# Performance work log

Hardware: AMD Instinct MI355X
Metric: run time of the kernel (lower is better)

Reference implementation:

```python
import jax, jax.numpy as jnp
import numpy as np

B, T, D, H = 4, 2048, 1024, 16
DK = D // H


def setup_inputs() -> dict:
    key = jax.random.key(0)
    ks = jax.random.split(key, 9)
    s = 1.0 / np.sqrt(D)
    x = jax.random.normal(ks[0], (B, T, D), dtype=jnp.float32)
    # causal mask: 1 = keep, 0 = masked (broadcastable over batch and heads)
    mask = jnp.tril(jnp.ones((T, T), dtype=jnp.int32))[None, None]
    params = {}
    for i, name in enumerate(['Wq', 'Wk', 'Wv', 'Wo']):
        params[name] = jax.random.normal(ks[1 + i], (D, D), dtype=jnp.float32) * s
    for i, name in enumerate(['bq', 'bk', 'bv', 'bo']):
        params[name] = jax.random.normal(ks[5 + i], (D,), dtype=jnp.float32) * s
    return {'x': x, 'mask': mask, **params}


def reference(x, mask, Wq, Wk, Wv, Wo, bq, bk, bv, bo):
    Bn, Tn, Dn = x.shape
    # torch.nn.Linear: y = x @ W.T + b
    q = (x @ Wq.T + bq).reshape(Bn, Tn, H, DK).transpose(0, 2, 1, 3)  # [B,H,T,dk]
    k = (x @ Wk.T + bk).reshape(Bn, Tn, H, DK).transpose(0, 2, 1, 3)
    v = (x @ Wv.T + bv).reshape(Bn, Tn, H, DK).transpose(0, 2, 1, 3)
    scores = jnp.einsum('bhqd,bhkd->bhqk', q, k) / jnp.sqrt(jnp.float32(DK))
    scores = jnp.where(mask == 0, -jnp.inf, scores)
    attn = jax.nn.softmax(scores, axis=-1)
    out = jnp.einsum('bhqk,bhkd->bhqd', attn, v)  # [B,H,T,dk]
    out = out.transpose(0, 2, 1, 3).reshape(Bn, Tn, Dn)
    return out @ Wo.T + bo
```

## Files before the change

kernel.cpp:

```cpp
#include <hip/hip_runtime.h>
#include <hip/hip_bf16.h>

#define T_LEN 2048
#define D_DIM 1024
#define H_NUM 16
#define DK 64

typedef unsigned short u16;
typedef __bf16 bf16x8 __attribute__((ext_vector_type(8)));
typedef float f32x4 __attribute__((ext_vector_type(4)));
typedef u16 u16x8 __attribute__((ext_vector_type(8)));
typedef u16 u16x4 __attribute__((ext_vector_type(4)));

#define AS1 __attribute__((address_space(1)))
#define AS3 __attribute__((address_space(3)))

#define QSCALE 0.18033688011112042f

__device__ __forceinline__ u16 f2bf(float f) {
    unsigned u = __builtin_bit_cast(unsigned, f);
    unsigned rounding = 0x7FFFu + ((u >> 16) & 1u);
    return (u16)((u + rounding) >> 16);
}

__global__ __launch_bounds__(256) void cvt_bf16(const float* __restrict__ in,
                                                u16* __restrict__ out, int n8) {
    int i = blockIdx.x * blockDim.x + threadIdx.x;
    if (i >= n8) return;
    const float4* p = (const float4*)in + (size_t)i * 2;
    float4 a = p[0], b = p[1];
    u16x8 r;
    r[0] = f2bf(a.x); r[1] = f2bf(a.y); r[2] = f2bf(a.z); r[3] = f2bf(a.w);
    r[4] = f2bf(b.x); r[5] = f2bf(b.y); r[6] = f2bf(b.z); r[7] = f2bf(b.w);
    *((u16x8*)out + i) = r;
}

__global__ __launch_bounds__(256) void cvt4_bf16(const float* __restrict__ a,
                                                 const float* __restrict__ b,
                                                 const float* __restrict__ c,
                                                 const float* __restrict__ d,
                                                 u16* __restrict__ out, int n8per) {
    int s = blockIdx.y;
    const float* src = s == 0 ? a : (s == 1 ? b : (s == 2 ? c : d));
    int i = blockIdx.x * blockDim.x + threadIdx.x;
    if (i >= n8per) return;
    const float4* p = (const float4*)src + (size_t)i * 2;
    float4 x = p[0], y = p[1];
    u16x8 r;
    r[0] = f2bf(x.x); r[1] = f2bf(x.y); r[2] = f2bf(x.z); r[3] = f2bf(x.w);
    r[4] = f2bf(y.x); r[5] = f2bf(y.y); r[6] = f2bf(y.z); r[7] = f2bf(y.w);
    *((u16x8*)(out + (size_t)s * n8per * 8) + i) = r;
}

template <int MODE>
__global__ __launch_bounds__(256) void gemm_bt(const u16* __restrict__ A,
                                               const u16* __restrict__ W,
                                               const float* __restrict__ b0,
                                               const float* __restrict__ b1,
                                               const float* __restrict__ b2,
                                               void* __restrict__ Cout,
                                               int M, int N, int K,
                                               int nxt, int nyt) {
    __shared__ u16 lA[2][128 * 32];
    __shared__ u16 lB[2][128 * 32];
    const int tid = threadIdx.x;
    const int w = tid >> 6, lane = tid & 63;

    const int bid = blockIdx.x;
    const int idx = bid >> 3;
    const int y = idx % nyt;
    const int x = (bid & 7) * (nxt >> 3) + idx / nyt;
    const int tm = x * 128;
    const int tn = y * 128;

    const int wm = (w >> 1) * 64, wn = (w & 1) * 64;
    const int kgrp = (lane >> 4) * 8;

    f32x4 acc[4][4] = {};

    auto stage = [&](int buf, int k0) {
#pragma unroll
        for (int r = 0; r < 2; ++r) {
            int c = r * 256 + tid;
            int row = c >> 2, col = (c & 3) * 8;
            __builtin_amdgcn_global_load_lds(
                (AS1 const void*)(A + (size_t)(tm + row) * K + k0 + col),
                (AS3 void*)(&lA[buf][(r * 256 + w * 64) * 8]), 16, 0, 0);
            __builtin_amdgcn_global_load_lds(
                (AS1 const void*)(W + (size_t)(tn + row) * K + k0 + col),
                (AS3 void*)(&lB[buf][(r * 256 + w * 64) * 8]), 16, 0, 0);
        }
    };

    stage(0, 0);
    asm volatile("s_waitcnt vmcnt(0)" ::: "memory");
    __syncthreads();

    const int niter = K >> 5;
    for (int it = 0; it < niter; ++it) {
        const int cur = it & 1;
        if (it + 1 < niter) stage(cur ^ 1, (it + 1) << 5);

        bf16x8 af[4], bfr[4];
#pragma unroll
        for (int i = 0; i < 4; ++i) {
            af[i]  = *(const bf16x8*)(&lA[cur][(wm + i * 16 + (lane & 15)) * 32 + kgrp]);
            bfr[i] = *(const bf16x8*)(&lB[cur][(wn + i * 16 + (lane & 15)) * 32 + kgrp]);
        }
#pragma unroll
        for (int mi = 0; mi < 4; ++mi)
#pragma unroll
            for (int ni = 0; ni < 4; ++ni)
                acc[mi][ni] = __builtin_amdgcn_mfma_f32_16x16x32_bf16(
                    af[mi], bfr[ni], acc[mi][ni], 0, 0, 0);

        asm volatile("s_waitcnt vmcnt(0)" ::: "memory");
        __syncthreads();
    }

    const int mtx = tn >> 10;
    const float* bp = mtx == 0 ? b0 : (mtx == 1 ? b1 : b2);
    const int crow0 = (lane >> 4) * 4;
    const int ccol = lane & 15;
#pragma unroll
    for (int mi = 0; mi < 4; ++mi) {
#pragma unroll
        for (int ni = 0; ni < 4; ++ni) {
            int n = tn + wn + ni * 16 + ccol;
            float bv = bp[n & 1023];
#pragma unroll
            for (int r = 0; r < 4; ++r) {
                int m = tm + wm + mi * 16 + crow0 + r;
                float val = acc[mi][ni][r] + bv;
                if (MODE == 0) {
                    ((float*)Cout)[(size_t)m * N + n] = val;
                } else {
                    if (mtx == 0) val *= QSCALE;
                    int b = m >> 11, t = m & (T_LEN - 1);
                    int nn = n & 1023;
                    int h = nn >> 6, d = nn & 63;
                    ((u16*)Cout)[(size_t)mtx * 8388608 +
                                 ((size_t)(b * H_NUM + h) * T_LEN + t) * DK + d] = f2bf(val);
                }
            }
        }
    }
}

__global__ __launch_bounds__(512) void attn_fwd(const u16* __restrict__ q,
                                                const u16* __restrict__ k,
                                                const u16* __restrict__ v,
                                                u16* __restrict__ o) {
    __shared__ u16 lK[2][64 * 64];
    __shared__ u16 lV[2][64 * 64];
    __shared__ u16 lP[8][16 * 72];
    __shared__ float lSc[8][16];

    const int tid = threadIdx.x, w = tid >> 6, lane = tid & 63;
    const int bid = blockIdx.x;
    const int idx = bid >> 3;
    const int bh = (bid & 7) * 8 + (idx & 7);
    const int bx = idx >> 3;

    const u16* qb = q + (size_t)bh * T_LEN * DK;
    const u16* kb = k + (size_t)bh * T_LEN * DK;
    const u16* vb = v + (size_t)bh * T_LEN * DK;

    const int g = lane >> 4;
    const int ccol = lane & 15;
    const int kg = tid >> 4;
    const int dc = tid & 15;
    const int wk = w - 4;
    const int b_ = bh >> 4, h_ = bh & 15;

    for (int seg = 0; seg < 2; ++seg) {
        const int qblk = seg ? (15 - bx) : bx;
        const int q0 = qblk * 128;
        const int ntiles = 2 * qblk + 2;
        const int rowbase = q0 + w * 16;
        const int myq = rowbase + ccol;

        bf16x8 qa[2];
#pragma unroll
        for (int kk = 0; kk < 2; ++kk)
            qa[kk] = *(const bf16x8*)(qb + (size_t)(rowbase + ccol) * DK + kk * 32 + g * 8);

        f32x4 oacc[4] = {};
        float mrow = -1e30f, lpart = 0.f;

        u16x4 vr[4];
        if (w >= 4) {
#pragma unroll
            for (int r2 = 0; r2 < 2; ++r2) {
                int c = r2 * 256 + wk * 64 + lane;
                int row = c >> 3, ch = c & 7;
                __builtin_amdgcn_global_load_lds(
                    (AS1 const void*)(kb + (size_t)row * DK + (ch ^ (row & 7)) * 8),
                    (AS3 void*)(&lK[0][(r2 * 256 + wk * 64) * 8]), 16, 0, 0);
            }
        } else {
#pragma unroll
            for (int i = 0; i < 4; ++i)
                vr[i] = *(const u16x4*)(vb + (size_t)(kg * 4 + i) * DK + dc * 4);
        }

        for (int kt = 0; kt < ntiles; ++kt) {
            const int bf = kt & 1;
            const int kv0 = kt << 6;
            asm volatile("s_waitcnt vmcnt(0)" ::: "memory");
            if (w < 4) {
#pragma unroll
                for (int j = 0; j < 4; ++j) {
                    int d = dc * 4 + j;
                    u16x4 t4;
                    t4[0] = vr[0][j]; t4[1] = vr[1][j]; t4[2] = vr[2][j]; t4[3] = vr[3][j];
                    *(u16x4*)(&lV[bf][d * 64 +
                        (((kg >> 1) ^ ((d >> 1) & 7)) * 8 + (kg & 1) * 4)]) = t4;
                }
            }
            __syncthreads();

            if (kt + 1 < ntiles) {
                const int kvn = (kt + 1) << 6;
                if (w >= 4) {
#pragma unroll
                    for (int r2 = 0; r2 < 2; ++r2) {
                        int c = r2 * 256 + wk * 64 + lane;
                        int row = c >> 3, ch = c & 7;
                        __builtin_amdgcn_global_load_lds(
                            (AS1 const void*)(kb + (size_t)(kvn + row) * DK + (ch ^ (row & 7)) * 8),
                            (AS3 void*)(&lK[bf ^ 1][(r2 * 256 + wk * 64) * 8]), 16, 0, 0);
                    }
                } else {
#pragma unroll
                    for (int i = 0; i < 4; ++i)
                        vr[i] = *(const u16x4*)(vb + (size_t)(kvn + kg * 4 + i) * DK + dc * 4);
                }
            }

            if (kv0 < rowbase + 16) {
                f32x4 sacc[4] = {};
                __builtin_amdgcn_s_setprio(1);
#pragma unroll
                for (int nt = 0; nt < 4; ++nt)
#pragma unroll
                    for (int kk = 0; kk < 2; ++kk) {
                        bf16x8 kf = *(const bf16x8*)(&lK[bf][(nt * 16 + ccol) * 64 +
                                                     (((kk * 4 + g) ^ (ccol & 7)) * 8)]);
                        sacc[nt] = __builtin_amdgcn_mfma_f32_16x16x32_bf16(
                            kf, qa[kk], sacc[nt], 0, 0, 0);
                    }
                __builtin_amdgcn_s_setprio(0);

                const bool full = (kv0 + 63) <= rowbase;
                float mx = -1e30f;
#pragma unroll
                for (int nt = 0; nt < 4; ++nt)
#pragma unroll
                    for (int r = 0; r < 4; ++r) {
                        float sv = sacc[nt][r];
                        if (!full && (kv0 + nt * 16 + g * 4 + r > myq)) sv = -1e30f;
                        sacc[nt][r] = sv;
                        mx = fmaxf(mx, sv);
                    }
                mx = fmaxf(mx, __shfl_xor(mx, 16));
                mx = fmaxf(mx, __shfl_xor(mx, 32));

                const bool skiprow = (mx <= mrow + 8.f);
                float mnew = skiprow ? mrow : mx;
                float p[4][4];
                float rsl = 0.f;
#pragma unroll
                for (int nt = 0; nt < 4; ++nt)
#pragma unroll
                    for (int r = 0; r < 4; ++r) {
                        float pv = __builtin_amdgcn_exp2f(sacc[nt][r] - mnew);
                        p[nt][r] = pv;
                        rsl += pv;
                    }
                float scal = skiprow ? 1.f : __builtin_amdgcn_exp2f(mrow - mnew);
                lpart = lpart * scal + rsl;
                mrow = mnew;

                if (lane < 16) lSc[w][lane] = scal;
#pragma unroll
                for (int nt = 0; nt < 4; ++nt) {
                    u16x4 t4;
                    t4[0] = f2bf(p[nt][0]); t4[1] = f2bf(p[nt][1]);
                    t4[2] = f2bf(p[nt][2]); t4[3] = f2bf(p[nt][3]);
                    *(u16x4*)(&lP[w][ccol * 72 + nt * 16 + g * 4]) = t4;
                }
                asm volatile("s_waitcnt lgkmcnt(0)" ::: "memory");

                f32x4 scalC = *(const f32x4*)(&lSc[w][g * 4]);
                if (__any(!skiprow)) {
#pragma unroll
                    for (int nt2 = 0; nt2 < 4; ++nt2)
#pragma unroll
                        for (int r = 0; r < 4; ++r) oacc[nt2][r] *= scalC[r];
                }

                bf16x8 pa[2];
#pragma unroll
                for (int kk2 = 0; kk2 < 2; ++kk2)
                    pa[kk2] = *(const bf16x8*)(&lP[w][ccol * 72 + kk2 * 32 + g * 8]);

                const int vsw = (ccol >> 1) & 7;
                __builtin_amdgcn_s_setprio(1);
#pragma unroll
                for (int nt2 = 0; nt2 < 4; ++nt2) {
#pragma unroll
                    for (int kk2 = 0; kk2 < 2; ++kk2) {
                        bf16x8 vf = *(const bf16x8*)(&lV[bf][(nt2 * 16 + ccol) * 64 +
                                                     (((kk2 * 4 + g) ^ vsw) * 8)]);
                        oacc[nt2] = __builtin_amdgcn_mfma_f32_16x16x32_bf16(
                            pa[kk2], vf, oacc[nt2], 0, 0, 0);
                    }
                }
                __builtin_amdgcn_s_setprio(0);
            }
        }
        __syncthreads();

        float rs = lpart;
        rs += __shfl_xor(rs, 16);
        rs += __shfl_xor(rs, 32);
        if (lane < 16) lSc[w][lane] = rs;
        asm volatile("s_waitcnt lgkmcnt(0)" ::: "memory");
        f32x4 rsC = *(const f32x4*)(&lSc[w][g * 4]);
#pragma unroll
        for (int r = 0; r < 4; ++r) {
            float inv = 1.0f / rsC[r];
            int trow = rowbase + g * 4 + r;
#pragma unroll
            for (int nt2 = 0; nt2 < 4; ++nt2) {
                float val = oacc[nt2][r] * inv;
                o[(size_t)(b_ * T_LEN + trow) * D_DIM + h_ * DK + nt2 * 16 + ccol] = f2bf(val);
            }
        }
        __syncthreads();
    }
}

extern "C" void kernel_launch(void* const* d_in, const int* in_sizes, int n_in,
                              void* d_out, int out_size, void* d_ws, size_t ws_size,
                              hipStream_t stream) {
    const float* x  = (const float*)d_in[0];
    const float* Wq = (const float*)d_in[2];
    const float* Wk = (const float*)d_in[3];
    const float* Wv = (const float*)d_in[4];
    const float* Wo = (const float*)d_in[5];
    const float* bq = (const float*)d_in[6];
    const float* bk = (const float*)d_in[7];
    const float* bv = (const float*)d_in[8];
    const float* bo = (const float*)d_in[9];

    char* ws = (char*)d_ws;
    u16* xb   = (u16*)(ws);
    u16* wqb  = (u16*)(ws + 16777216);
    u16* wob  = (u16*)(ws + 23068672);
    u16* qws  = (u16*)(ws + 25165824);
    u16* kws  = (u16*)(ws + 41943040);
    u16* vws  = (u16*)(ws + 58720256);
    u16* attnb = xb;

    cvt_bf16<<<4096, 256, 0, stream>>>(x, xb, 1048576);
    cvt4_bf16<<<dim3(512, 4), 256, 0, stream>>>(Wq, Wk, Wv, Wo, wqb, 131072);

    gemm_bt<1><<<1536, 256, 0, stream>>>(xb, wqb, bq, bk, bv, qws, 8192, 3072, 1024, 64, 24);

    attn_fwd<<<512, 512, 0, stream>>>(qws, kws, vws, attnb);

    gemm_bt<0><<<512, 256, 0, stream>>>(attnb, wob, bo, bo, bo, d_out, 8192, 1024, 1024, 64, 8);
}
```

Baseline: 291.8 us.

## Add dedicated 256x256-tile QKV GEMM with swizzled LDS and deeper prefetch

Replaces the generic 128x128 QKV projection GEMM with a dedicated 512-thread kernel that computes 256x256 output tiles. It uses direct global-to-LDS loads, an XOR-swizzled LDS layout, and a multi-stage pipeline of half-k sub-tiles interleaved with MFMA phases under raised wave priority. The goal is more operand reuse per LDS byte, fewer bank conflicts, and better overlap of loads with compute. The trade-offs are more registers (128 accumulators per thread) and only 384 blocks, which may leave CUs underfilled. The output-projection GEMM is reduced to a plain fp32-output version with the mode template removed.

```diff
diff --git a/kernel.cpp b/kernel.cpp
--- a/kernel.cpp
+++ b/kernel.cpp
@@ -52,13 +52,116 @@
     *((u16x8*)(out + (size_t)s * n8per * 8) + i) = r;
 }
 
-template <int MODE>
+__global__ __launch_bounds__(512) void gemm_qkv(const u16* __restrict__ A,
+                                                const u16* __restrict__ W,
+                                                const float* __restrict__ b0,
+                                                const float* __restrict__ b1,
+                                                const float* __restrict__ b2,
+                                                u16* __restrict__ Cout) {
+    __shared__ u16 L[2][4][8192];
+    const int tid = threadIdx.x, w = tid >> 6, lane = tid & 63;
+    const int sw = (blockIdx.x & 7) * 48 + (blockIdx.x >> 3);
+    const int xm = sw / 12, yn = sw % 12;
+    const int tm = xm * 256, tn = yn * 256;
+    const int wr = w >> 2, wc = w & 3;
+    const int g = lane >> 4, ccol = lane & 15;
+    const int gsw = (g ^ ((ccol >> 1) & 3)) * 8;
+    const int K = 1024, NT = 16;
+
+    const u16* Ab = A + (size_t)tm * K;
+    const u16* Wb = W + (size_t)tn * K;
+
+    const int srow = w * 16 + (lane >> 2);
+    const int skk  = (((lane & 3) ^ ((lane >> 3) & 3))) * 8;
+
+    f32x4 acc[8][4] = {};
+
+    auto stage = [&](const u16* gb, int k0, int ksub, u16* reg) {
+#pragma unroll
+        for (int h2 = 0; h2 < 2; ++h2) {
+            __builtin_amdgcn_global_load_lds(
+                (AS1 const void*)(gb + (size_t)(h2 * 128 + srow) * K + k0 + ksub * 32 + skk),
+                (AS3 void*)(reg + h2 * 4096 + w * 512), 16, 0, 0);
+        }
+    };
+
+    stage(Ab, 0, 0, L[0][0]);
+    stage(Wb, 0, 0, L[0][2]);
+    stage(Ab, 0, 1, L[0][1]);
+    stage(Wb, 0, 1, L[0][3]);
+    stage(Ab, 64, 0, L[1][0]);
+    stage(Wb, 64, 0, L[1][2]);
+    asm volatile("s_waitcnt vmcnt(4)" ::: "memory");
+    __builtin_amdgcn_s_barrier();
+
+    bf16x8 bfr[4];
+    for (int t = 0; t < NT; ++t) {
+        const int par = t & 1;
+        u16* LA0 = L[par][0]; u16* LA1 = L[par][1];
+        u16* LB0 = L[par][2]; u16* LB1 = L[par][3];
+#pragma unroll
+        for (int p = 0; p < 4; ++p) {
+            const int mh = (p & 1) * 4;
+            u16* LAk = (p >> 1) ? LA1 : LA0;
+            u16* LBk = (p >> 1) ? LB1 : LB0;
+            bf16x8 af[4];
+#pragma unroll
+            for (int i = 0; i < 4; ++i)
+                af[i] = *(const bf16x8*)(LAk + (wr * 128 + (mh + i) * 16 + ccol) * 32 + gsw);
+            if ((p & 1) == 0) {
+#pragma unroll
+                for (int i = 0; i < 4; ++i)
+                    bfr[i] = *(const bf16x8*)(LBk + (wc * 64 + i * 16 + ccol) * 32 + gsw);
+            }
+            if (p == 0)      { if (t + 1 < NT) stage(Ab, (t + 1) * 64, 1, L[(t + 1) & 1][1]); }
+            else if (p == 1) { if (t + 1 < NT) stage(Wb, (t + 1) * 64, 1, L[(t + 1) & 1][3]); }
+            else if (p == 2) { if (t + 2 < NT) stage(Ab, (t + 2) * 64, 0, L[par][0]); }
+            else {
+                if (t + 2 < NT) stage(Wb, (t + 2) * 64, 0, L[par][2]);
+                if (t < NT - 2) asm volatile("s_waitcnt vmcnt(4)" ::: "memory");
+                else            asm volatile("s_waitcnt vmcnt(0)" ::: "memory");
+            }
+            __builtin_amdgcn_s_barrier();
+            asm volatile("s_waitcnt lgkmcnt(0)" ::: "memory");
+            __builtin_amdgcn_sched_barrier(0);
+            __builtin_amdgcn_s_setprio(1);
+#pragma unroll
+            for (int ni = 0; ni < 4; ++ni)
+#pragma unroll
+                for (int mi = 0; mi < 4; ++mi)
+                    acc[mh + mi][ni] = __builtin_amdgcn_mfma_f32_16x16x32_bf16(
+                        af[mi], bfr[ni], acc[mh + mi][ni], 0, 0, 0);
+            __builtin_amdgcn_s_setprio(0);
+            __builtin_amdgcn_s_barrier();
+        }
+    }
+
+    const int mtx = yn >> 2;
+    const float* bp = mtx == 0 ? b0 : (mtx == 1 ? b1 : b2);
+#pragma unroll
+    for (int mi = 0; mi < 8; ++mi) {
+#pragma unroll
+        for (int ni = 0; ni < 4; ++ni) {
+            int nn = (tn + wc * 64 + ni * 16 + ccol) & 1023;
+            float bv = bp[nn];
+            int h = nn >> 6, d = nn & 63;
+#pragma unroll
+            for (int r = 0; r < 4; ++r) {
+                int m = tm + wr * 128 + mi * 16 + g * 4 + r;
+                float val = acc[mi][ni][r] + bv;
+                if (mtx == 0) val *= QSCALE;
+                int b = m >> 11, tt = m & (T_LEN - 1);
+                Cout[(size_t)mtx * 8388608 +
+                     ((size_t)(b * H_NUM + h) * T_LEN + tt) * DK + d] = f2bf(val);
+            }
+        }
+    }
+}
+
 __global__ __launch_bounds__(256) void gemm_bt(const u16* __restrict__ A,
                                                const u16* __restrict__ W,
                                                const float* __restrict__ b0,
-                                               const float* __restrict__ b1,
-                                               const float* __restrict__ b2,
-                                               void* __restrict__ Cout,
+                                               float* __restrict__ Cout,
                                                int M, int N, int K,
                                                int nxt, int nyt) {
     __shared__ u16 lA[2][128 * 32];
@@ -118,8 +221,6 @@
         __syncthreads();
     }
 
-    const int mtx = tn >> 10;
-    const float* bp = mtx == 0 ? b0 : (mtx == 1 ? b1 : b2);
     const int crow0 = (lane >> 4) * 4;
     const int ccol = lane & 15;
 #pragma unroll
@@ -127,21 +228,11 @@
 #pragma unroll
         for (int ni = 0; ni < 4; ++ni) {
             int n = tn + wn + ni * 16 + ccol;
-            float bv = bp[n & 1023];
+            float bv = b0[n & 1023];
 #pragma unroll
             for (int r = 0; r < 4; ++r) {
                 int m = tm + wm + mi * 16 + crow0 + r;
-                float val = acc[mi][ni][r] + bv;
-                if (MODE == 0) {
-                    ((float*)Cout)[(size_t)m * N + n] = val;
-                } else {
-                    if (mtx == 0) val *= QSCALE;
-                    int b = m >> 11, t = m & (T_LEN - 1);
-                    int nn = n & 1023;
-                    int h = nn >> 6, d = nn & 63;
-                    ((u16*)Cout)[(size_t)mtx * 8388608 +
-                                 ((size_t)(b * H_NUM + h) * T_LEN + t) * DK + d] = f2bf(val);
-                }
+                Cout[(size_t)m * N + n] = acc[mi][ni][r] + bv;
             }
         }
     }
@@ -367,9 +458,9 @@
     cvt_bf16<<<4096, 256, 0, stream>>>(x, xb, 1048576);
     cvt4_bf16<<<dim3(512, 4), 256, 0, stream>>>(Wq, Wk, Wv, Wo, wqb, 131072);
 
-    gemm_bt<1><<<1536, 256, 0, stream>>>(xb, wqb, bq, bk, bv, qws, 8192, 3072, 1024, 64, 24);
+    gemm_qkv<<<384, 512, 0, stream>>>(xb, wqb, bq, bk, bv, qws);
 
     attn_fwd<<<512, 512, 0, stream>>>(qws, kws, vws, attnb);
 
-    gemm_bt<0><<<512, 256, 0, stream>>>(attnb, wob, bo, bo, bo, d_out, 8192, 1024, 1024, 64, 8);
-}
+    gemm_bt<<<512, 256, 0, stream>>>(attnb, wob, bo, (float*)d_out, 8192, 1024, 1024, 64, 8);
+}
```

Result: faster. 273.5 us (-6.3%).

## Rewrite projection GEMMs with 128x256 tiles, deeper LDS pipeline and swizzle

Applied to the files above, without the earlier changes.

Replaces the 128x128, 256-thread GEMM with a 512-thread kernel computing 128x256 tiles. Each K step of 64 is split into two 32-wide phases, and loads are kept about three stages ahead using counted vmcnt waits. LDS reads are XOR-swizzled to cut bank conflicts, and MFMA priority is raised. The attention kernel also switches P conversion to the hardware packed bf16 convert instruction. The cost is more LDS per block, which lowers occupancy, and hardcoded K and N dimensions.

```diff
diff --git a/kernel.cpp b/kernel.cpp
--- a/kernel.cpp
+++ b/kernel.cpp
@@ -52,76 +52,91 @@
     *((u16x8*)(out + (size_t)s * n8per * 8) + i) = r;
 }
 
-template <int MODE>
-__global__ __launch_bounds__(256) void gemm_bt(const u16* __restrict__ A,
+template <int MODE, int NYT>
+__global__ __launch_bounds__(512) void gemm_bp(const u16* __restrict__ A,
                                                const u16* __restrict__ W,
                                                const float* __restrict__ b0,
                                                const float* __restrict__ b1,
                                                const float* __restrict__ b2,
-                                               void* __restrict__ Cout,
-                                               int M, int N, int K,
-                                               int nxt, int nyt) {
-    __shared__ u16 lA[2][128 * 32];
-    __shared__ u16 lB[2][128 * 32];
-    const int tid = threadIdx.x;
-    const int w = tid >> 6, lane = tid & 63;
-
-    const int bid = blockIdx.x;
-    const int idx = bid >> 3;
-    const int y = idx % nyt;
-    const int x = (bid & 7) * (nxt >> 3) + idx / nyt;
-    const int tm = x * 128;
-    const int tn = y * 128;
-
-    const int wm = (w >> 1) * 64, wn = (w & 1) * 64;
-    const int kgrp = (lane >> 4) * 8;
+                                               void* __restrict__ Cout) {
+    __shared__ u16 LA[2][2][4096];
+    __shared__ u16 LB[2][2][8192];
+    const int tid = threadIdx.x, w = tid >> 6, lane = tid & 63;
+    const int loc = blockIdx.x >> 3;
+    const int xm = (blockIdx.x & 7) * 8 + loc / NYT;
+    const int yn = loc % NYT;
+    const int tm = xm * 128, tn = yn * 256;
+    const int wr = w >> 2, wc = w & 3;
+    const int wm = wr * 64, wn = wc * 64;
+    const int g = lane >> 4, ccol = lane & 15;
+    const int gsw = (g ^ ((ccol >> 1) & 3)) * 8;
+    const int NT = 16;
+
+    const int srow = tid >> 2;
+    const int skk = ((tid & 3) ^ ((tid >> 3) & 3)) * 8;
 
     f32x4 acc[4][4] = {};
 
-    auto stage = [&](int buf, int k0) {
-#pragma unroll
-        for (int r = 0; r < 2; ++r) {
-            int c = r * 256 + tid;
-            int row = c >> 2, col = (c & 3) * 8;
+    auto stageA = [&](int par, int kk, int k0) {
+        __builtin_amdgcn_global_load_lds(
+            (AS1 const void*)(A + (size_t)(tm + srow) * 1024 + k0 + kk * 32 + skk),
+            (AS3 void*)(&LA[par][kk][w * 512]), 16, 0, 0);
+    };
+    auto stageB = [&](int par, int kk, int k0) {
+#pragma unroll
+        for (int h = 0; h < 2; ++h)
             __builtin_amdgcn_global_load_lds(
-                (AS1 const void*)(A + (size_t)(tm + row) * K + k0 + col),
-                (AS3 void*)(&lA[buf][(r * 256 + w * 64) * 8]), 16, 0, 0);
-            __builtin_amdgcn_global_load_lds(
-                (AS1 const void*)(W + (size_t)(tn + row) * K + k0 + col),
-                (AS3 void*)(&lB[buf][(r * 256 + w * 64) * 8]), 16, 0, 0);
-        }
+                (AS1 const void*)(W + (size_t)(tn + h * 128 + srow) * 1024 + k0 + kk * 32 + skk),
+                (AS3 void*)(&LB[par][kk][h * 4096 + w * 512]), 16, 0, 0);
     };
 
-    stage(0, 0);
-    asm volatile("s_waitcnt vmcnt(0)" ::: "memory");
-    __syncthreads();
-
-    const int niter = K >> 5;
-    for (int it = 0; it < niter; ++it) {
-        const int cur = it & 1;
-        if (it + 1 < niter) stage(cur ^ 1, (it + 1) << 5);
-
-        bf16x8 af[4], bfr[4];
-#pragma unroll
-        for (int i = 0; i < 4; ++i) {
-            af[i]  = *(const bf16x8*)(&lA[cur][(wm + i * 16 + (lane & 15)) * 32 + kgrp]);
-            bfr[i] = *(const bf16x8*)(&lB[cur][(wn + i * 16 + (lane & 15)) * 32 + kgrp]);
-        }
-#pragma unroll
-        for (int mi = 0; mi < 4; ++mi)
-#pragma unroll
-            for (int ni = 0; ni < 4; ++ni)
-                acc[mi][ni] = __builtin_amdgcn_mfma_f32_16x16x32_bf16(
-                    af[mi], bfr[ni], acc[mi][ni], 0, 0, 0);
-
-        asm volatile("s_waitcnt vmcnt(0)" ::: "memory");
-        __syncthreads();
+    stageA(0, 0, 0);  stageB(0, 0, 0);
+    stageA(0, 1, 0);  stageB(0, 1, 0);
+    stageA(1, 0, 64); stageB(1, 0, 64);
+
+    for (int t = 0; t < NT; ++t) {
+        const int par = t & 1;
+#pragma unroll
+        for (int ph = 0; ph < 2; ++ph) {
+            if (ph == 0) {
+                if (t + 1 < NT) { stageA(par ^ 1, 1, (t + 1) * 64); stageB(par ^ 1, 1, (t + 1) * 64); }
+            } else {
+                if (t + 2 < NT) { stageA(par, 0, (t + 2) * 64); stageB(par, 0, (t + 2) * 64); }
+            }
+            if (ph == 0) {
+                if (t < NT - 1) asm volatile("s_waitcnt vmcnt(9)" ::: "memory");
+                else            asm volatile("s_waitcnt vmcnt(3)" ::: "memory");
+            } else {
+                if (t < NT - 2)      asm volatile("s_waitcnt vmcnt(9)" ::: "memory");
+                else if (t == NT - 2) asm volatile("s_waitcnt vmcnt(6)" ::: "memory");
+                else                 asm volatile("s_waitcnt vmcnt(0)" ::: "memory");
+            }
+            __builtin_amdgcn_s_barrier();
+
+            const u16* LAp = LA[par][ph];
+            const u16* LBp = LB[par][ph];
+            bf16x8 af[4], bfr[4];
+#pragma unroll
+            for (int i = 0; i < 4; ++i) {
+                af[i]  = *(const bf16x8*)(LAp + (wm + i * 16 + ccol) * 32 + gsw);
+                bfr[i] = *(const bf16x8*)(LBp + (wn + i * 16 + ccol) * 32 + gsw);
+            }
+            asm volatile("s_waitcnt lgkmcnt(0)" ::: "memory");
+            __builtin_amdgcn_sched_barrier(0);
+            __builtin_amdgcn_s_setprio(1);
+#pragma unroll
+            for (int mi = 0; mi < 4; ++mi)
+#pragma unroll
+                for (int ni = 0; ni < 4; ++ni)
+                    acc[mi][ni] = __builtin_amdgcn_mfma_f32_16x16x32_bf16(
+                        af[mi], bfr[ni], acc[mi][ni], 0, 0, 0);
+            __builtin_amdgcn_s_setprio(0);
+            __builtin_amdgcn_s_barrier();
+        }
     }
 
-    const int mtx = tn >> 10;
-    const float* bp = mtx == 0 ? b0 : (mtx == 1 ? b1 : b2);
-    const int crow0 = (lane >> 4) * 4;
-    const int ccol = lane & 15;
+    const int mtx = yn >> 2;
+    const float* bp = MODE == 0 ? b0 : (mtx == 0 ? b0 : (mtx == 1 ? b1 : b2));
 #pragma unroll
     for (int mi = 0; mi < 4; ++mi) {
 #pragma unroll
@@ -130,17 +145,17 @@
             float bv = bp[n & 1023];
 #pragma unroll
             for (int r = 0; r < 4; ++r) {
-                int m = tm + wm + mi * 16 + crow0 + r;
+                int m = tm + wm + mi * 16 + g * 4 + r;
                 float val = acc[mi][ni][r] + bv;
                 if (MODE == 0) {
-                    ((float*)Cout)[(size_t)m * N + n] = val;
+                    ((float*)Cout)[(size_t)m * 1024 + n] = val;
                 } else {
                     if (mtx == 0) val *= QSCALE;
-                    int b = m >> 11, t = m & (T_LEN - 1);
                     int nn = n & 1023;
                     int h = nn >> 6, d = nn & 63;
+                    int b = m >> 11, tt = m & (T_LEN - 1);
                     ((u16*)Cout)[(size_t)mtx * 8388608 +
-                                 ((size_t)(b * H_NUM + h) * T_LEN + t) * DK + d] = f2bf(val);
+                                 ((size_t)(b * H_NUM + h) * T_LEN + tt) * DK + d] = f2bf(val);
                 }
             }
         }
@@ -285,10 +300,11 @@
                 if (lane < 16) lSc[w][lane] = scal;
 #pragma unroll
                 for (int nt = 0; nt < 4; ++nt) {
-                    u16x4 t4;
-                    t4[0] = f2bf(p[nt][0]); t4[1] = f2bf(p[nt][1]);
-                    t4[2] = f2bf(p[nt][2]); t4[3] = f2bf(p[nt][3]);
-                    *(u16x4*)(&lP[w][ccol * 72 + nt * 16 + g * 4]) = t4;
+                    unsigned w0, w1;
+                    asm("v_cvt_pk_bf16_f32 %0, %1, %2" : "=v"(w0) : "v"(p[nt][0]), "v"(p[nt][1]));
+                    asm("v_cvt_pk_bf16_f32 %0, %1, %2" : "=v"(w1) : "v"(p[nt][2]), "v"(p[nt][3]));
+                    uint2 pk; pk.x = w0; pk.y = w1;
+                    *(uint2*)(&lP[w][ccol * 72 + nt * 16 + g * 4]) = pk;
                 }
                 asm volatile("s_waitcnt lgkmcnt(0)" ::: "memory");
 
@@ -367,9 +383,9 @@
     cvt_bf16<<<4096, 256, 0, stream>>>(x, xb, 1048576);
     cvt4_bf16<<<dim3(512, 4), 256, 0, stream>>>(Wq, Wk, Wv, Wo, wqb, 131072);
 
-    gemm_bt<1><<<1536, 256, 0, stream>>>(xb, wqb, bq, bk, bv, qws, 8192, 3072, 1024, 64, 24);
+    gemm_bp<1, 12><<<768, 512, 0, stream>>>(xb, wqb, bq, bk, bv, qws);
 
     attn_fwd<<<512, 512, 0, stream>>>(qws, kws, vws, attnb);
 
-    gemm_bt<0><<<512, 256, 0, stream>>>(attnb, wob, bo, bo, bo, d_out, 8192, 1024, 1024, 64, 8);
-}
+    gemm_bp<0, 4><<<256, 512, 0, stream>>>(attnb, wob, bo, bo, bo, d_out);
+}
```

New measurement: 299.7 us. 1.03x slower.
